# Optimization experiments

Hardware: AMD Instinct MI355X
Metric: run time of the kernel (lower is better)

The kernel has to match this reference:

```python
import jax, jax.numpy as jnp
import numpy as np

B, T, D, H = 64, 512, 1024, 1024


def setup_inputs() -> dict:
    key = jax.random.key(0)
    k1, k2, k3, k4, k5, k6 = jax.random.split(key, 6)
    feature = jax.random.normal(k1, (B, T, D), dtype=jnp.float32)
    # lengths sorted descending (pack_padded_sequence enforce_sorted=True); max == T
    lens = jnp.sort(jax.random.randint(k2, (B,), 1, T + 1))[::-1]
    seq_len = lens.at[0].set(T).astype(jnp.int32)
    s = 1.0 / np.sqrt(H)
    W_ih = jax.random.uniform(k3, (4 * H, D), jnp.float32, -s, s)
    W_hh = jax.random.uniform(k4, (4 * H, H), jnp.float32, -s, s)
    b_ih = jax.random.uniform(k5, (4 * H,), jnp.float32, -s, s)
    b_hh = jax.random.uniform(k6, (4 * H,), jnp.float32, -s, s)
    return {"feature": feature, "W_ih": W_ih, "W_hh": W_hh,
            "b_ih": b_ih, "b_hh": b_hh, "seq_len": seq_len}


def _lstm(feature, W_ih, W_hh, b_ih, b_hh, seq_len):
    Bb, Tt, _ = feature.shape
    Hh = W_hh.shape[1]
    # precompute input contributions for all steps: [B,T,4H] -> [T,B,4H]
    x_gates = jnp.einsum('btd,gd->btg', feature, W_ih) + (b_ih + b_hh)
    x_gates = jnp.transpose(x_gates, (1, 0, 2))
    # valid-step mask per timestep: [T,B]
    mask = (jnp.arange(Tt)[:, None] < seq_len[None, :])

    def step(carry, inp):
        h, c = carry
        xg, m = inp  # [B,4H], [B]
        gates = xg + h @ W_hh.T
        i, f, g, o = jnp.split(gates, 4, axis=-1)  # PyTorch gate order i,f,g,o
        i = jax.nn.sigmoid(i)
        f = jax.nn.sigmoid(f)
        g = jnp.tanh(g)
        o = jax.nn.sigmoid(o)
        c_new = f * c + i * g
        h_new = o * jnp.tanh(c_new)
        m = m[:, None]
        h = jnp.where(m, h_new, h)  # packed semantics: state frozen past length
        c = jnp.where(m, c_new, c)
        out = jnp.where(m, h_new, 0.0)  # pad_packed_sequence pads with zeros
        return (h, c), out

    h0 = jnp.zeros((Bb, Hh), feature.dtype)
    c0 = jnp.zeros((Bb, Hh), feature.dtype)
    _, outs = jax.lax.scan(step, (h0, c0), (x_gates, mask))
    return jnp.transpose(outs, (1, 0, 2))  # [B,T,H]


def reference(feature, W_ih, W_hh, b_ih, b_hh, seq_len):
    return _lstm(feature, W_ih, W_hh, b_ih, b_hh, seq_len)
```

## Files before the change

kernel.cpp:

```cpp
#include <hip/hip_runtime.h>
#include <stdint.h>

typedef unsigned short ushort_t;
typedef unsigned long long ull_t;
typedef __attribute__((ext_vector_type(8))) short short8;
typedef __attribute__((ext_vector_type(2))) unsigned long long ull2;
typedef __attribute__((ext_vector_type(4))) float f32x4;
typedef __attribute__((ext_vector_type(4))) float float4v;
typedef __attribute__((ext_vector_type(4))) unsigned short ushort4v;
typedef __attribute__((ext_vector_type(4))) unsigned int uint4v;

#define NB 64
#define NT 512
#define ND 1024
#define NHH 1024
#define NG 4096

__device__ __forceinline__ ushort_t f2bf(float x) {
    uint32_t u = __builtin_bit_cast(uint32_t, x);
    u += 0x7fffu + ((u >> 16) & 1u);
    return (ushort_t)(u >> 16);
}
__device__ __forceinline__ float bf2f(ushort_t b) {
    uint32_t u = ((uint32_t)b) << 16;
    return __builtin_bit_cast(float, u);
}
__device__ __forceinline__ float fsigmoid(float x) { return 1.f / (1.f + __expf(-x)); }
__device__ __forceinline__ float ftanh(float x) {
    float ax = __builtin_fabsf(x);
    float e = __expf(-2.f * ax);
    float r = (1.f - e) / (1.f + e);
    return x < 0.f ? -r : r;
}
__device__ __forceinline__ void xg_store(float* p, float v) { *p = v; }
__device__ __forceinline__ void xg_store(ushort_t* p, float v) { *p = f2bf(v); }
__device__ __forceinline__ float4v xg_load4(const float4v* p) { return *p; }
__device__ __forceinline__ float4v xg_load4(const ushort4v* p) {
    ushort4v u = *p;
    float4v r = { bf2f(u[0]), bf2f(u[1]), bf2f(u[2]), bf2f(u[3]) };
    return r;
}
__device__ __forceinline__ void async_cp16(const ushort_t* g, ushort_t* s) {
    __builtin_amdgcn_global_load_lds(
        (const __attribute__((address_space(1))) uint32_t*)g,
        (__attribute__((address_space(3))) uint32_t*)s, 16, 0, 0);
}

__global__ __launch_bounds__(256) void k_prep(
    const float* __restrict__ feat, const float* __restrict__ wih,
    const float* __restrict__ whh,
    ushort_t* __restrict__ featb, ushort_t* __restrict__ wihb,
    ushort_t* __restrict__ whhb, ushort_t* __restrict__ hbuf,
    int* __restrict__ cnt)
{
    const size_t NF = (size_t)NB * NT * ND / 4;
    const size_t NW = (size_t)NG * ND / 4;
    const size_t NHB = (size_t)2 * 65536 * 2 / 16;
    size_t total = NF + 2 * NW + NHB;
    size_t stride = (size_t)gridDim.x * blockDim.x;
    for (size_t i = (size_t)blockIdx.x * blockDim.x + threadIdx.x; i < total; i += stride) {
        if (i < NF) {
            float4v v = ((const float4v*)feat)[i];
            ushort4v o = { f2bf(v[0]), f2bf(v[1]), f2bf(v[2]), f2bf(v[3]) };
            ((ushort4v*)featb)[i] = o;
        } else if (i < NF + NW) {
            size_t j = i - NF;
            size_t row = j >> 8, kc = j & 255;
            size_t rowp = ((row & 1023) << 2) | (row >> 10);
            float4v v = ((const float4v*)wih)[j];
            ushort4v o = { f2bf(v[0]), f2bf(v[1]), f2bf(v[2]), f2bf(v[3]) };
            ((ushort4v*)wihb)[rowp * 256 + kc] = o;
        } else if (i < NF + 2 * NW) {
            size_t j = i - NF - NW;
            float4v v = ((const float4v*)whh)[j];
            ushort4v o = { f2bf(v[0]), f2bf(v[1]), f2bf(v[2]), f2bf(v[3]) };
            ((ushort4v*)whhb)[j] = o;
        } else {
            size_t j = i - NF - 2 * NW;
            uint4v z = { 0u, 0u, 0u, 0u };
            ((uint4v*)hbuf)[j] = z;
        }
    }
    if (blockIdx.x < 16) cnt[blockIdx.x * 256 + threadIdx.x] = 0;
}

template <typename XGT>
__global__ __launch_bounds__(256) void k_gemm(
    const ushort_t* __restrict__ Ab,
    const ushort_t* __restrict__ Bb,
    const float* __restrict__ bih, const float* __restrict__ bhh,
    const int* __restrict__ slenp, XGT* __restrict__ xg)
{
    int bid = blockIdx.x;
    int panel = bid >> 8;
    int qq = bid & 255;
    int mt = (panel << 3) | (qq & 7);
    int nt = qq >> 3;
    int m0 = mt << 7, n0 = nt << 7;
    int b = m0 >> 9;
    int t0 = m0 & 511;
    int sl = slenp[b];
    if (t0 >= sl) return;

    __shared__ short8 ldsA8[1024];
    __shared__ short8 ldsB8[1024];
    ushort_t* ldsA = (ushort_t*)ldsA8;
    ushort_t* ldsB = (ushort_t*)ldsB8;
    const ushort_t* gA = Ab + (size_t)m0 * 1024;
    const ushort_t* gB = Bb + (size_t)n0 * 1024;

    int tid = threadIdx.x;
    int wave = tid >> 6, lane = tid & 63;
    int wm = (wave >> 1) << 6;
    int wn = (wave & 1) << 6;
    int fl = lane & 15, fq = lane >> 4;

    f32x4 acc[4][4];
#pragma unroll
    for (int i = 0; i < 4; i++)
#pragma unroll
        for (int j = 0; j < 4; j++) { f32x4 z = {0.f, 0.f, 0.f, 0.f}; acc[i][j] = z; }

    int srow_[4], skb_[4];
#pragma unroll
    for (int u = 0; u < 4; u++) {
        int s = u * 256 + tid;
        srow_[u] = s >> 3;
        skb_[u] = (s & 7) ^ (srow_[u] & 7);
    }

    for (int k0 = 0; k0 < 1024; k0 += 64) {
        if (k0) __syncthreads();
#pragma unroll
        for (int u = 0; u < 4; u++) {
            ushort_t* sa = ldsA + (size_t)(u * 256 + wave * 64) * 8;
            ushort_t* sb = ldsB + (size_t)(u * 256 + wave * 64) * 8;
            async_cp16(gA + (size_t)srow_[u] * 1024 + k0 + skb_[u] * 8, sa);
            async_cp16(gB + (size_t)srow_[u] * 1024 + k0 + skb_[u] * 8, sb);
        }
        __syncthreads();
#pragma unroll
        for (int ks = 0; ks < 2; ks++) {
            int kc = ks * 4 + fq;
            short8 af[4], bf[4];
#pragma unroll
            for (int i = 0; i < 4; i++) {
                int ra = wm + i * 16 + fl;
                int rb = wn + i * 16 + fl;
                af[i] = ldsA8[ra * 8 + (kc ^ (ra & 7))];
                bf[i] = ldsB8[rb * 8 + (kc ^ (rb & 7))];
            }
#pragma unroll
            for (int i = 0; i < 4; i++)
#pragma unroll
                for (int j = 0; j < 4; j++)
                    acc[i][j] = __builtin_amdgcn_mfma_f32_16x16x32_bf16(af[i], bf[j], acc[i][j], 0, 0, 0);
        }
    }
#pragma unroll
    for (int j = 0; j < 4; j++) {
        int rp = n0 + wn + j * 16 + fl;
        int bi = ((rp & 3) << 10) | (rp >> 2);
        float bv = bih[bi] + bhh[bi];
#pragma unroll
        for (int i = 0; i < 4; i++) {
#pragma unroll
            for (int r = 0; r < 4; r++) {
                int m = wm + i * 16 + fq * 4 + r;
                int t = t0 + m;
                if (t < sl)
                    xg_store(&xg[((size_t)t * 64 + b) * 4096 + rp], acc[i][j][r] + bv);
            }
        }
    }
}

template <typename XG4>
__global__ __launch_bounds__(256, 1) void k_rec(
    const ushort_t* __restrict__ whhb, const XG4* __restrict__ xg4,
    const int* __restrict__ slenp, ushort_t* __restrict__ hbuf,
    float* __restrict__ out, int* __restrict__ cnt)
{
    const int tid = threadIdx.x;
    const int ks = tid >> 6, lane = tid & 63;
    const int wg = blockIdx.x;
    const int mb = wg >> 6;
    const int mem = wg & 63;
    const int j0 = mem << 4;
    const int nn = lane & 15, q = lane >> 4;

    short8 wfrag[4][8];
    {
        const short8* w8 = (const short8*)whhb;
#pragma unroll
        for (int g = 0; g < 4; g++) {
            const short8* wp = w8 + (size_t)(g * NHH + j0 + nn) * 128 + ks * 32;
#pragma unroll
            for (int u = 0; u < 8; u++) wfrag[g][u] = wp[u * 4 + q];
        }
    }
    const int eb = tid >> 4, ej = tid & 15;
    const int b_g = (mb << 4) + eb;
    const int j_g = j0 + ej;
    const int slen = slenp[b_g];
    const int blk_len = slenp[mb << 4];
    const int ab = (mb << 4) + nn;

    int* flags = cnt + mb * 1024;
    int* myflag = flags + mem * 16 + ks * 4;
    const int* pollp = flags + ((ks * 16 + (lane >> 2)) * 16) + (lane & 3) * 4;

    __shared__ float red[4 * 16 * 84];

    float c_st = 0.f, h_st = 0.f, hv_prev = 0.f;
    float4v xv = { 0.f, 0.f, 0.f, 0.f };
    if (0 < slen) xv = xg_load4(&xg4[(size_t)b_g * 1024 + j_g]);

#pragma unroll 1
    for (int t = 0; t < blk_len; ++t) {
        if (t > 0) out[((size_t)b_g * NT + (t - 1)) * 1024 + j_g] = hv_prev;
        float4v nxv = { 0.f, 0.f, 0.f, 0.f };
        if (t + 1 < slen) nxv = xg_load4(&xg4[((size_t)(t + 1) * 64 + b_g) * 1024 + j_g]);

        if (t > 0) {
            while (true) {
                int f = __hip_atomic_load(pollp, __ATOMIC_RELAXED, __HIP_MEMORY_SCOPE_AGENT);
                if (__ballot(f >= t) == ~0ull) break;
            }
            asm volatile("" ::: "memory");
        }

        const ull_t* hb8 = (const ull_t*)(hbuf + (size_t)(t & 1) * 65536);
        ull_t raw[16];
#pragma unroll
        for (int u = 0; u < 8; u++) {
            size_t ch = ((size_t)((ks * 32 + u * 4 + q) * 64 + ab)) * 2;
            raw[2 * u]     = __hip_atomic_load(&hb8[ch],     __ATOMIC_RELAXED, __HIP_MEMORY_SCOPE_AGENT);
            raw[2 * u + 1] = __hip_atomic_load(&hb8[ch + 1], __ATOMIC_RELAXED, __HIP_MEMORY_SCOPE_AGENT);
        }
        f32x4 acc[4];
#pragma unroll
        for (int g = 0; g < 4; g++) { f32x4 z = {0.f, 0.f, 0.f, 0.f}; acc[g] = z; }
#pragma unroll
        for (int u = 0; u < 8; u++) {
            ull2 p; p[0] = raw[2 * u]; p[1] = raw[2 * u + 1];
            short8 af = __builtin_bit_cast(short8, p);
#pragma unroll
            for (int g = 0; g < 4; g++)
                acc[g] = __builtin_amdgcn_mfma_f32_16x16x32_bf16(af, wfrag[g][u], acc[g], 0, 0, 0);
        }
        __syncthreads();
#pragma unroll
        for (int g = 0; g < 4; g++)
            *(f32x4*)&red[g * 1344 + nn * 84 + ks * 20 + q * 4] = acc[g];
        __syncthreads();

        float hv = 0.f;
        if (t < slen) {
            float s[4];
#pragma unroll
            for (int g = 0; g < 4; g++) {
                const float* rp = &red[g * 1344 + ej * 84 + eb];
                s[g] = (rp[0] + rp[20]) + (rp[40] + rp[60]);
            }
            float ip = s[0] + xv[0];
            float fp = s[1] + xv[1];
            float gp = s[2] + xv[2];
            float op = s[3] + xv[3];
            float i_s = fsigmoid(ip), f_s = fsigmoid(fp);
            float g_t = ftanh(gp), o_s = fsigmoid(op);
            float cn = __builtin_fmaf(f_s, c_st, i_s * g_t);
            c_st = cn;
            h_st = o_s * ftanh(cn);
            hv = h_st;
        }
        hv_prev = hv;
        __hip_atomic_store(&hbuf[(size_t)((t + 1) & 1) * 65536 +
                                 (size_t)((j_g >> 3) * 64 + b_g) * 8 + (j_g & 7)],
                           f2bf(h_st), __ATOMIC_RELAXED, __HIP_MEMORY_SCOPE_AGENT);
        xv = nxv;
        asm volatile("s_waitcnt vmcnt(0)" ::: "memory");
        if (lane == 0)
            __hip_atomic_store(myflag, t + 1, __ATOMIC_RELAXED, __HIP_MEMORY_SCOPE_AGENT);
    }
    out[((size_t)b_g * NT + (blk_len - 1)) * 1024 + j_g] = hv_prev;
    for (int t = blk_len; t < NT; ++t)
        out[((size_t)b_g * NT + t) * 1024 + j_g] = 0.f;
}

extern "C" void kernel_launch(void* const* d_in, const int* in_sizes, int n_in,
                              void* d_out, int out_size, void* d_ws, size_t ws_size,
                              hipStream_t stream)
{
    const float* feat = (const float*)d_in[0];
    const float* wih  = (const float*)d_in[1];
    const float* whh  = (const float*)d_in[2];
    const float* bih  = (const float*)d_in[3];
    const float* bhh  = (const float*)d_in[4];
    const int*   sl   = (const int*)d_in[5];
    float* out = (float*)d_out;
    char* ws = (char*)d_ws;

    size_t off = 0;
    auto take = [&](size_t bytes) -> size_t {
        size_t o = off; off += (bytes + 255) & ~(size_t)255; return o;
    };
    size_t o_featb = take((size_t)NB * NT * ND * 2);
    size_t o_wihb  = take((size_t)NG * ND * 2);
    size_t o_whhb  = take((size_t)NG * ND * 2);
    size_t o_hbuf  = take((size_t)2 * 65536 * 2);
    size_t o_cnt   = take(16384);
    size_t o_xg    = off;

    ushort_t* featb = (ushort_t*)(ws + o_featb);
    ushort_t* wihb  = (ushort_t*)(ws + o_wihb);
    ushort_t* whhb  = (ushort_t*)(ws + o_whhb);
    ushort_t* hbuf  = (ushort_t*)(ws + o_hbuf);
    int* cnt        = (int*)(ws + o_cnt);

    k_prep<<<2048, 256, 0, stream>>>(feat, wih, whh, featb, wihb, whhb, hbuf, cnt);

    size_t xg_elems = (size_t)NT * NB * NG;
    bool f32xg = (o_xg + xg_elems * 4) <= ws_size;
    if (f32xg) {
        float* xg = (float*)(ws + o_xg);
        k_gemm<float><<<8192, 256, 0, stream>>>(featb, wihb, bih, bhh, sl, xg);
        k_rec<float4v><<<256, 256, 0, stream>>>(whhb, (const float4v*)xg, sl, hbuf, out, cnt);
    } else {
        ushort_t* xg = (ushort_t*)(ws + o_xg);
        k_gemm<ushort_t><<<8192, 256, 0, stream>>>(featb, wihb, bih, bhh, sl, xg);
        k_rec<ushort4v><<<256, 256, 0, stream>>>(whhb, (const ushort4v*)xg, sl, hbuf, out, cnt);
    }
}
```

Baseline: 2.119 ms.

## Halve recurrent workgroups, stage h in LDS, and simplify flag polling

The recurrent kernel now runs 128 workgroups of 512 threads instead of 256 of 256. Each workgroup covers 32 hidden units across two 16-column wave groups, so fewer groups take part in the per-step global barrier. The hidden state is loaded from global memory once per workgroup with coalesced loads, staged in LDS and shared by all eight waves, instead of each wave doing its own strided global loads. Flag polling becomes a per-thread 64-bit load with a bounded spin instead of a wavefront ballot. Output stores are written in the same step rather than deferred, and the spin guard risks silently wrong results if it ever times out.

```diff
diff --git a/kernel.cpp b/kernel.cpp
--- a/kernel.cpp
+++ b/kernel.cpp
@@ -176,83 +176,100 @@
 }
 
 template <typename XG4>
-__global__ __launch_bounds__(256, 1) void k_rec(
+__global__ __launch_bounds__(512, 2) void k_rec(
     const ushort_t* __restrict__ whhb, const XG4* __restrict__ xg4,
     const int* __restrict__ slenp, ushort_t* __restrict__ hbuf,
     float* __restrict__ out, int* __restrict__ cnt)
 {
     const int tid = threadIdx.x;
-    const int ks = tid >> 6, lane = tid & 63;
     const int wg = blockIdx.x;
-    const int mb = wg >> 6;
-    const int mem = wg & 63;
-    const int j0 = mem << 4;
+    const int mb = wg >> 5;
+    const int mem = wg & 31;
+    const int j0 = mem << 5;
+    const int w = tid >> 6, lane = tid & 63;
+    const int jb = w >> 2, ks = w & 3;
     const int nn = lane & 15, q = lane >> 4;
 
     short8 wfrag[4][8];
     {
         const short8* w8 = (const short8*)whhb;
+        const int jw = j0 + (jb << 4);
 #pragma unroll
         for (int g = 0; g < 4; g++) {
-            const short8* wp = w8 + (size_t)(g * NHH + j0 + nn) * 128 + ks * 32;
+            const short8* wp = w8 + (size_t)(g * NHH + jw + nn) * 128 + ks * 32;
 #pragma unroll
             for (int u = 0; u < 8; u++) wfrag[g][u] = wp[u * 4 + q];
         }
     }
-    const int eb = tid >> 4, ej = tid & 15;
-    const int b_g = (mb << 4) + eb;
-    const int j_g = j0 + ej;
+
+    const int j_t = tid & 31, b_t = tid >> 5;
+    const int b_g = (mb << 4) + b_t;
+    const int j_gl = j0 + j_t;
     const int slen = slenp[b_g];
     const int blk_len = slenp[mb << 4];
-    const int ab = (mb << 4) + nn;
-
-    int* flags = cnt + mb * 1024;
-    int* myflag = flags + mem * 16 + ks * 4;
-    const int* pollp = flags + ((ks * 16 + (lane >> 2)) * 16) + (lane & 3) * 4;
-
-    __shared__ float red[4 * 16 * 84];
-
-    float c_st = 0.f, h_st = 0.f, hv_prev = 0.f;
+
+    const int jc = tid >> 2, q4 = tid & 3;
+    const size_t src_base = ((size_t)(jc * 64 + (mb << 4) + (q4 << 2))) << 1;
+
+    int* flags = cnt + mb * 256;
+    const ull_t* flagsU = (const ull_t*)flags;
+    const int pollU = (jc >> 2) * 4 + q4;
+    const int myflag = mem * 8 + w;
+
+    __shared__ short8 A_lds8[2048];
+    __shared__ float red[4 * 2176];
+
+    float c_st = 0.f, h_st = 0.f;
     float4v xv = { 0.f, 0.f, 0.f, 0.f };
-    if (0 < slen) xv = xg_load4(&xg4[(size_t)b_g * 1024 + j_g]);
+    if (0 < slen) xv = xg_load4(&xg4[(size_t)b_g * 1024 + j_gl]);
 
 #pragma unroll 1
     for (int t = 0; t < blk_len; ++t) {
-        if (t > 0) out[((size_t)b_g * NT + (t - 1)) * 1024 + j_g] = hv_prev;
         float4v nxv = { 0.f, 0.f, 0.f, 0.f };
-        if (t + 1 < slen) nxv = xg_load4(&xg4[((size_t)(t + 1) * 64 + b_g) * 1024 + j_g]);
+        if (t + 1 < slen) nxv = xg_load4(&xg4[((size_t)(t + 1) * 64 + b_g) * 1024 + j_gl]);
 
         if (t > 0) {
+            int guard = 0;
             while (true) {
-                int f = __hip_atomic_load(pollp, __ATOMIC_RELAXED, __HIP_MEMORY_SCOPE_AGENT);
-                if (__ballot(f >= t) == ~0ull) break;
+                ull_t f = __hip_atomic_load(&flagsU[pollU], __ATOMIC_RELAXED, __HIP_MEMORY_SCOPE_AGENT);
+                if ((int)(uint32_t)f >= t && (int)(uint32_t)(f >> 32) >= t) break;
+                if (++guard > (1 << 20)) break;
             }
             asm volatile("" ::: "memory");
         }
-
-        const ull_t* hb8 = (const ull_t*)(hbuf + (size_t)(t & 1) * 65536);
-        ull_t raw[16];
+        const ull_t* src = (const ull_t*)(hbuf + (size_t)(t & 1) * 65536) + src_base;
+        ull_t v[8];
+#pragma unroll
+        for (int u2 = 0; u2 < 8; u2++)
+            v[u2] = __hip_atomic_load(&src[u2], __ATOMIC_RELAXED, __HIP_MEMORY_SCOPE_AGENT);
+#pragma unroll
+        for (int i = 0; i < 4; i++) {
+            ull2 p; p[0] = v[2 * i]; p[1] = v[2 * i + 1];
+            A_lds8[tid * 4 + i] = __builtin_bit_cast(short8, p);
+        }
+        __syncthreads();
+
+        f32x4 acc0 = { 0.f, 0.f, 0.f, 0.f };
+        f32x4 acc1 = acc0, acc2 = acc0, acc3 = acc0;
 #pragma unroll
         for (int u = 0; u < 8; u++) {
-            size_t ch = ((size_t)((ks * 32 + u * 4 + q) * 64 + ab)) * 2;
-            raw[2 * u]     = __hip_atomic_load(&hb8[ch],     __ATOMIC_RELAXED, __HIP_MEMORY_SCOPE_AGENT);
-            raw[2 * u + 1] = __hip_atomic_load(&hb8[ch + 1], __ATOMIC_RELAXED, __HIP_MEMORY_SCOPE_AGENT);
-        }
-        f32x4 acc[4];
-#pragma unroll
-        for (int g = 0; g < 4; g++) { f32x4 z = {0.f, 0.f, 0.f, 0.f}; acc[g] = z; }
-#pragma unroll
-        for (int u = 0; u < 8; u++) {
-            ull2 p; p[0] = raw[2 * u]; p[1] = raw[2 * u + 1];
-            short8 af = __builtin_bit_cast(short8, p);
-#pragma unroll
-            for (int g = 0; g < 4; g++)
-                acc[g] = __builtin_amdgcn_mfma_f32_16x16x32_bf16(af, wfrag[g][u], acc[g], 0, 0, 0);
-        }
-        __syncthreads();
-#pragma unroll
-        for (int g = 0; g < 4; g++)
-            *(f32x4*)&red[g * 1344 + nn * 84 + ks * 20 + q * 4] = acc[g];
+            short8 af = A_lds8[(ks * 32 + u * 4 + q) * 16 + nn];
+            acc0 = __builtin_amdgcn_mfma_f32_16x16x32_bf16(af, wfrag[0][u], acc0, 0, 0, 0);
+            acc1 = __builtin_amdgcn_mfma_f32_16x16x32_bf16(af, wfrag[1][u], acc1, 0, 0, 0);
+            acc2 = __builtin_amdgcn_mfma_f32_16x16x32_bf16(af, wfrag[2][u], acc2, 0, 0, 0);
+            acc3 = __builtin_amdgcn_mfma_f32_16x16x32_bf16(af, wfrag[3][u], acc3, 0, 0, 0);
+        }
+        {
+            const int jj = (jb << 4) + nn;
+#pragma unroll
+            for (int r = 0; r < 4; r++) {
+                int bo = jj * 68 + (q * 4 + r) * 4 + ks;
+                red[0 * 2176 + bo] = acc0[r];
+                red[1 * 2176 + bo] = acc1[r];
+                red[2 * 2176 + bo] = acc2[r];
+                red[3 * 2176 + bo] = acc3[r];
+            }
+        }
         __syncthreads();
 
         float hv = 0.f;
@@ -260,8 +277,8 @@
             float s[4];
 #pragma unroll
             for (int g = 0; g < 4; g++) {
-                const float* rp = &red[g * 1344 + ej * 84 + eb];
-                s[g] = (rp[0] + rp[20]) + (rp[40] + rp[60]);
+                f32x4 pv = *(const f32x4*)&red[g * 2176 + j_t * 68 + b_t * 4];
+                s[g] = (pv[0] + pv[1]) + (pv[2] + pv[3]);
             }
             float ip = s[0] + xv[0];
             float fp = s[1] + xv[1];
@@ -274,18 +291,17 @@
             h_st = o_s * ftanh(cn);
             hv = h_st;
         }
-        hv_prev = hv;
         __hip_atomic_store(&hbuf[(size_t)((t + 1) & 1) * 65536 +
-                                 (size_t)((j_g >> 3) * 64 + b_g) * 8 + (j_g & 7)],
+                                 (size_t)((j_gl >> 3) * 64 + b_g) * 8 + (j_gl & 7)],
                            f2bf(h_st), __ATOMIC_RELAXED, __HIP_MEMORY_SCOPE_AGENT);
-        xv = nxv;
         asm volatile("s_waitcnt vmcnt(0)" ::: "memory");
         if (lane == 0)
-            __hip_atomic_store(myflag, t + 1, __ATOMIC_RELAXED, __HIP_MEMORY_SCOPE_AGENT);
-    }
-    out[((size_t)b_g * NT + (blk_len - 1)) * 1024 + j_g] = hv_prev;
-    for (int t = blk_len; t < NT; ++t)
-        out[((size_t)b_g * NT + t) * 1024 + j_g] = 0.f;
+            __hip_atomic_store(&flags[myflag], t + 1, __ATOMIC_RELAXED, __HIP_MEMORY_SCOPE_AGENT);
+        out[((size_t)b_g * NT + t) * 1024 + j_gl] = hv;
+        xv = nxv;
+    }
+    for (int t2 = blk_len; t2 < NT; ++t2)
+        out[((size_t)b_g * NT + t2) * 1024 + j_gl] = 0.f;
 }
 
 extern "C" void kernel_launch(void* const* d_in, const int* in_sizes, int n_in,
@@ -325,10 +341,10 @@
     if (f32xg) {
         float* xg = (float*)(ws + o_xg);
         k_gemm<float><<<8192, 256, 0, stream>>>(featb, wihb, bih, bhh, sl, xg);
-        k_rec<float4v><<<256, 256, 0, stream>>>(whhb, (const float4v*)xg, sl, hbuf, out, cnt);
+        k_rec<float4v><<<128, 512, 0, stream>>>(whhb, (const float4v*)xg, sl, hbuf, out, cnt);
     } else {
         ushort_t* xg = (ushort_t*)(ws + o_xg);
         k_gemm<ushort_t><<<8192, 256, 0, stream>>>(featb, wihb, bih, bhh, sl, xg);
-        k_rec<ushort4v><<<256, 256, 0, stream>>>(whhb, (const ushort4v*)xg, sl, hbuf, out, cnt);
-    }
-}
+        k_rec<ushort4v><<<128, 512, 0, stream>>>(whhb, (const ushort4v*)xg, sl, hbuf, out, cnt);
+    }
+}
```

Result: slower. 2.903 ms (+37.0%).

## Fuse input-projection GEMM and recurrence into one persistent kernel with readiness flags

Applied to the files above, without the earlier changes.

Merges the xg GEMM and the recurrent LSTM kernel into a single launch. The first 256 blocks run the recurrence, and the remaining blocks compute GEMM tiles reordered by time window, bumping per-tile ready counters. The recurrence blocks poll those counters before consuming each 128-step window, so the serial recurrence can start before the full input projection finishes. This risks deadlock or contention if the recurrence blocks occupy CUs the GEMM blocks need, which the code guards with bounded spin loops. It also depends on block scheduling order and adds atomic stores on the GEMM output.

```diff
diff --git a/kernel.cpp b/kernel.cpp
--- a/kernel.cpp
+++ b/kernel.cpp
@@ -32,8 +32,12 @@
     float r = (1.f - e) / (1.f + e);
     return x < 0.f ? -r : r;
 }
-__device__ __forceinline__ void xg_store(float* p, float v) { *p = v; }
-__device__ __forceinline__ void xg_store(ushort_t* p, float v) { *p = f2bf(v); }
+__device__ __forceinline__ void xg_astore(float* p, float v) {
+    __hip_atomic_store(p, v, __ATOMIC_RELAXED, __HIP_MEMORY_SCOPE_AGENT);
+}
+__device__ __forceinline__ void xg_astore(ushort_t* p, float v) {
+    __hip_atomic_store(p, f2bf(v), __ATOMIC_RELAXED, __HIP_MEMORY_SCOPE_AGENT);
+}
 __device__ __forceinline__ float4v xg_load4(const float4v* p) { return *p; }
 __device__ __forceinline__ float4v xg_load4(const ushort4v* p) {
     ushort4v u = *p;
@@ -84,103 +88,116 @@
     if (blockIdx.x < 16) cnt[blockIdx.x * 256 + threadIdx.x] = 0;
 }
 
-template <typename XGT>
-__global__ __launch_bounds__(256) void k_gemm(
+template <typename XGT, typename XG4>
+__global__ __launch_bounds__(256, 2) void k_fused(
     const ushort_t* __restrict__ Ab,
     const ushort_t* __restrict__ Bb,
     const float* __restrict__ bih, const float* __restrict__ bhh,
-    const int* __restrict__ slenp, XGT* __restrict__ xg)
+    const int* __restrict__ slenp,
+    XGT* xg, const ushort_t* __restrict__ whhb,
+    ushort_t* hbuf, float* __restrict__ out, int* cnt)
 {
-    int bid = blockIdx.x;
-    int panel = bid >> 8;
-    int qq = bid & 255;
-    int mt = (panel << 3) | (qq & 7);
-    int nt = qq >> 3;
-    int m0 = mt << 7, n0 = nt << 7;
-    int b = m0 >> 9;
-    int t0 = m0 & 511;
-    int sl = slenp[b];
-    if (t0 >= sl) return;
-
-    __shared__ short8 ldsA8[1024];
-    __shared__ short8 ldsB8[1024];
-    ushort_t* ldsA = (ushort_t*)ldsA8;
-    ushort_t* ldsB = (ushort_t*)ldsB8;
-    const ushort_t* gA = Ab + (size_t)m0 * 1024;
-    const ushort_t* gB = Bb + (size_t)n0 * 1024;
-
-    int tid = threadIdx.x;
-    int wave = tid >> 6, lane = tid & 63;
-    int wm = (wave >> 1) << 6;
-    int wn = (wave & 1) << 6;
-    int fl = lane & 15, fq = lane >> 4;
-
-    f32x4 acc[4][4];
-#pragma unroll
-    for (int i = 0; i < 4; i++)
-#pragma unroll
-        for (int j = 0; j < 4; j++) { f32x4 z = {0.f, 0.f, 0.f, 0.f}; acc[i][j] = z; }
-
-    int srow_[4], skb_[4];
-#pragma unroll
-    for (int u = 0; u < 4; u++) {
-        int s = u * 256 + tid;
-        srow_[u] = s >> 3;
-        skb_[u] = (s & 7) ^ (srow_[u] & 7);
-    }
-
-    for (int k0 = 0; k0 < 1024; k0 += 64) {
-        if (k0) __syncthreads();
+    extern __shared__ char smem[];
+    int* rdy = cnt + 1024;
+
+    if (blockIdx.x >= 256) {
+        int bid2 = blockIdx.x - 256;
+        int w = bid2 >> 11;
+        int qq = bid2 & 2047;
+        int pp = qq >> 8;
+        int q2 = qq & 255;
+        int bl = (pp << 3) | (q2 & 7);
+        int nt = q2 >> 3;
+        int mt = (bl << 2) | w;
+        int m0 = mt << 7, n0 = nt << 7;
+        int b = bl;
+        int t0 = w << 7;
+        int sl = slenp[b];
+        if (t0 >= sl) {
+            if (threadIdx.x == 0)
+                __hip_atomic_fetch_add(&rdy[mt], 1, __ATOMIC_RELAXED, __HIP_MEMORY_SCOPE_AGENT);
+            return;
+        }
+
+        short8* ldsA8 = (short8*)smem;
+        short8* ldsB8 = (short8*)(smem + 16384);
+        ushort_t* ldsA = (ushort_t*)ldsA8;
+        ushort_t* ldsB = (ushort_t*)ldsB8;
+        const ushort_t* gA = Ab + (size_t)m0 * 1024;
+        const ushort_t* gB = Bb + (size_t)n0 * 1024;
+
+        int tid = threadIdx.x;
+        int wave = tid >> 6, lane = tid & 63;
+        int wm = (wave >> 1) << 6;
+        int wn = (wave & 1) << 6;
+        int fl = lane & 15, fq = lane >> 4;
+
+        f32x4 acc[4][4];
+#pragma unroll
+        for (int i = 0; i < 4; i++)
+#pragma unroll
+            for (int j = 0; j < 4; j++) { f32x4 z = {0.f, 0.f, 0.f, 0.f}; acc[i][j] = z; }
+
+        int srow_[4], skb_[4];
 #pragma unroll
         for (int u = 0; u < 4; u++) {
-            ushort_t* sa = ldsA + (size_t)(u * 256 + wave * 64) * 8;
-            ushort_t* sb = ldsB + (size_t)(u * 256 + wave * 64) * 8;
-            async_cp16(gA + (size_t)srow_[u] * 1024 + k0 + skb_[u] * 8, sa);
-            async_cp16(gB + (size_t)srow_[u] * 1024 + k0 + skb_[u] * 8, sb);
-        }
+            int s = u * 256 + tid;
+            srow_[u] = s >> 3;
+            skb_[u] = (s & 7) ^ (srow_[u] & 7);
+        }
+
+        for (int k0 = 0; k0 < 1024; k0 += 64) {
+            if (k0) __syncthreads();
+#pragma unroll
+            for (int u = 0; u < 4; u++) {
+                ushort_t* sa = ldsA + (size_t)(u * 256 + wave * 64) * 8;
+                ushort_t* sb = ldsB + (size_t)(u * 256 + wave * 64) * 8;
+                async_cp16(gA + (size_t)srow_[u] * 1024 + k0 + skb_[u] * 8, sa);
+                async_cp16(gB + (size_t)srow_[u] * 1024 + k0 + skb_[u] * 8, sb);
+            }
+            __syncthreads();
+#pragma unroll
+            for (int ks = 0; ks < 2; ks++) {
+                int kc = ks * 4 + fq;
+                short8 af[4], bf[4];
+#pragma unroll
+                for (int i = 0; i < 4; i++) {
+                    int ra = wm + i * 16 + fl;
+                    int rb = wn + i * 16 + fl;
+                    af[i] = ldsA8[ra * 8 + (kc ^ (ra & 7))];
+                    bf[i] = ldsB8[rb * 8 + (kc ^ (rb & 7))];
+                }
+#pragma unroll
+                for (int i = 0; i < 4; i++)
+#pragma unroll
+                    for (int j = 0; j < 4; j++)
+                        acc[i][j] = __builtin_amdgcn_mfma_f32_16x16x32_bf16(af[i], bf[j], acc[i][j], 0, 0, 0);
+            }
+        }
+#pragma unroll
+        for (int j = 0; j < 4; j++) {
+            int rp = n0 + wn + j * 16 + fl;
+            int bi = ((rp & 3) << 10) | (rp >> 2);
+            float bv = bih[bi] + bhh[bi];
+#pragma unroll
+            for (int i = 0; i < 4; i++) {
+#pragma unroll
+                for (int r = 0; r < 4; r++) {
+                    int m = wm + i * 16 + fq * 4 + r;
+                    int t = t0 + m;
+                    if (t < sl)
+                        xg_astore(&xg[((size_t)t * 64 + b) * 4096 + rp], acc[i][j][r] + bv);
+                }
+            }
+        }
+        asm volatile("s_waitcnt vmcnt(0)" ::: "memory");
         __syncthreads();
-#pragma unroll
-        for (int ks = 0; ks < 2; ks++) {
-            int kc = ks * 4 + fq;
-            short8 af[4], bf[4];
-#pragma unroll
-            for (int i = 0; i < 4; i++) {
-                int ra = wm + i * 16 + fl;
-                int rb = wn + i * 16 + fl;
-                af[i] = ldsA8[ra * 8 + (kc ^ (ra & 7))];
-                bf[i] = ldsB8[rb * 8 + (kc ^ (rb & 7))];
-            }
-#pragma unroll
-            for (int i = 0; i < 4; i++)
-#pragma unroll
-                for (int j = 0; j < 4; j++)
-                    acc[i][j] = __builtin_amdgcn_mfma_f32_16x16x32_bf16(af[i], bf[j], acc[i][j], 0, 0, 0);
-        }
-    }
-#pragma unroll
-    for (int j = 0; j < 4; j++) {
-        int rp = n0 + wn + j * 16 + fl;
-        int bi = ((rp & 3) << 10) | (rp >> 2);
-        float bv = bih[bi] + bhh[bi];
-#pragma unroll
-        for (int i = 0; i < 4; i++) {
-#pragma unroll
-            for (int r = 0; r < 4; r++) {
-                int m = wm + i * 16 + fq * 4 + r;
-                int t = t0 + m;
-                if (t < sl)
-                    xg_store(&xg[((size_t)t * 64 + b) * 4096 + rp], acc[i][j][r] + bv);
-            }
-        }
-    }
-}
-
-template <typename XG4>
-__global__ __launch_bounds__(256, 1) void k_rec(
-    const ushort_t* __restrict__ whhb, const XG4* __restrict__ xg4,
-    const int* __restrict__ slenp, ushort_t* __restrict__ hbuf,
-    float* __restrict__ out, int* __restrict__ cnt)
-{
+        if (threadIdx.x == 0)
+            __hip_atomic_fetch_add(&rdy[mt], 1, __ATOMIC_RELAXED, __HIP_MEMORY_SCOPE_AGENT);
+        return;
+    }
+
+    const XG4* xg4 = (const XG4*)xg;
     const int tid = threadIdx.x;
     const int ks = tid >> 6, lane = tid & 63;
     const int wg = blockIdx.x;
@@ -206,26 +223,42 @@
     const int blk_len = slenp[mb << 4];
     const int ab = (mb << 4) + nn;
 
-    int* flags = cnt + mb * 1024;
-    int* myflag = flags + mem * 16 + ks * 4;
-    const int* pollp = flags + ((ks * 16 + (lane >> 2)) * 16) + (lane & 3) * 4;
-
-    __shared__ float red[4 * 16 * 84];
+    int* flags = cnt + mb * 256;
+    int* myflag = flags + mem * 4 + ks;
+    const int* fp = flags + (ks * 16 + (lane >> 2)) * 4 + (lane & 3);
+
+    const int ridx = ((mb << 4) + (lane & 15)) << 2;
+    auto waitwin = [&](int w2) {
+        int guard = 0;
+        while (true) {
+            int f = __hip_atomic_load(&rdy[ridx + w2], __ATOMIC_RELAXED, __HIP_MEMORY_SCOPE_AGENT);
+            if (__ballot(f >= 32) == ~0ull) break;
+            if (++guard > (1 << 20)) break;
+            __builtin_amdgcn_s_sleep(8);
+        }
+        asm volatile("" ::: "memory");
+    };
+
+    float* red = (float*)smem;
 
     float c_st = 0.f, h_st = 0.f, hv_prev = 0.f;
+    waitwin(0);
     float4v xv = { 0.f, 0.f, 0.f, 0.f };
     if (0 < slen) xv = xg_load4(&xg4[(size_t)b_g * 1024 + j_g]);
 
 #pragma unroll 1
     for (int t = 0; t < blk_len; ++t) {
         if (t > 0) out[((size_t)b_g * NT + (t - 1)) * 1024 + j_g] = hv_prev;
+        if (t + 1 < blk_len && ((t + 1) & 127) == 0) waitwin((t + 1) >> 7);
         float4v nxv = { 0.f, 0.f, 0.f, 0.f };
         if (t + 1 < slen) nxv = xg_load4(&xg4[((size_t)(t + 1) * 64 + b_g) * 1024 + j_g]);
 
         if (t > 0) {
+            int guard = 0;
             while (true) {
-                int f = __hip_atomic_load(pollp, __ATOMIC_RELAXED, __HIP_MEMORY_SCOPE_AGENT);
+                int f = __hip_atomic_load(fp, __ATOMIC_RELAXED, __HIP_MEMORY_SCOPE_AGENT);
                 if (__ballot(f >= t) == ~0ull) break;
+                if (++guard > (1 << 20)) break;
             }
             asm volatile("" ::: "memory");
         }
@@ -264,10 +297,10 @@
                 s[g] = (rp[0] + rp[20]) + (rp[40] + rp[60]);
             }
             float ip = s[0] + xv[0];
-            float fp = s[1] + xv[1];
+            float fpv = s[1] + xv[1];
             float gp = s[2] + xv[2];
             float op = s[3] + xv[3];
-            float i_s = fsigmoid(ip), f_s = fsigmoid(fp);
+            float i_s = fsigmoid(ip), f_s = fsigmoid(fpv);
             float g_t = ftanh(gp), o_s = fsigmoid(op);
             float cn = __builtin_fmaf(f_s, c_st, i_s * g_t);
             c_st = cn;
@@ -278,10 +311,10 @@
         __hip_atomic_store(&hbuf[(size_t)((t + 1) & 1) * 65536 +
                                  (size_t)((j_g >> 3) * 64 + b_g) * 8 + (j_g & 7)],
                            f2bf(h_st), __ATOMIC_RELAXED, __HIP_MEMORY_SCOPE_AGENT);
-        xv = nxv;
         asm volatile("s_waitcnt vmcnt(0)" ::: "memory");
         if (lane == 0)
             __hip_atomic_store(myflag, t + 1, __ATOMIC_RELAXED, __HIP_MEMORY_SCOPE_AGENT);
+        xv = nxv;
     }
     out[((size_t)b_g * NT + (blk_len - 1)) * 1024 + j_g] = hv_prev;
     for (int t = blk_len; t < NT; ++t)
@@ -324,11 +357,11 @@
     bool f32xg = (o_xg + xg_elems * 4) <= ws_size;
     if (f32xg) {
         float* xg = (float*)(ws + o_xg);
-        k_gemm<float><<<8192, 256, 0, stream>>>(featb, wihb, bih, bhh, sl, xg);
-        k_rec<float4v><<<256, 256, 0, stream>>>(whhb, (const float4v*)xg, sl, hbuf, out, cnt);
+        k_fused<float, float4v><<<8448, 256, 32768, stream>>>(
+            featb, wihb, bih, bhh, sl, xg, whhb, hbuf, out, cnt);
     } else {
         ushort_t* xg = (ushort_t*)(ws + o_xg);
-        k_gemm<ushort_t><<<8192, 256, 0, stream>>>(featb, wihb, bih, bhh, sl, xg);
-        k_rec<ushort4v><<<256, 256, 0, stream>>>(whhb, (const ushort4v*)xg, sl, hbuf, out, cnt);
-    }
-}
+        k_fused<ushort_t, ushort4v><<<8448, 256, 32768, stream>>>(
+            featb, wihb, bih, bhh, sl, xg, whhb, hbuf, out, cnt);
+    }
+}
```

Measured after the change: 2.668 ms. 25.9% more time.

## Replace flag-based step barrier with parity bits embedded in bf16 hidden state

Applied to the files above, without the earlier changes.

The separate per-workgroup flag array and its polling barrier are removed. Instead, the lowest mantissa bit of each bf16 hidden-state element carries a step-parity tag, and readers spin on the data words themselves until every loaded chunk shows the expected parity. This drops the vmcnt wait, the flag store and the separate flag-poll round trip each timestep, so consumers can start as soon as their specific inputs arrive. In exchange the hidden state loses one mantissa bit of precision, the second buffer is initialised with the opposite parity, and a guard counter can break out of the spin and silently use stale data.

```diff
diff --git a/kernel.cpp b/kernel.cpp
--- a/kernel.cpp
+++ b/kernel.cpp
@@ -77,7 +77,8 @@
             ((ushort4v*)whhb)[j] = o;
         } else {
             size_t j = i - NF - 2 * NW;
-            uint4v z = { 0u, 0u, 0u, 0u };
+            uint32_t fill = (j < 8192) ? 0u : 0x00010001u;
+            uint4v z = { fill, fill, fill, fill };
             ((uint4v*)hbuf)[j] = z;
         }
     }
@@ -181,6 +182,7 @@
     const int* __restrict__ slenp, ushort_t* __restrict__ hbuf,
     float* __restrict__ out, int* __restrict__ cnt)
 {
+    (void)cnt;
     const int tid = threadIdx.x;
     const int ks = tid >> 6, lane = tid & 63;
     const int wg = blockIdx.x;
@@ -206,11 +208,9 @@
     const int blk_len = slenp[mb << 4];
     const int ab = (mb << 4) + nn;
 
-    int* flags = cnt + mb * 1024;
-    int* myflag = flags + mem * 16 + ks * 4;
-    const int* pollp = flags + ((ks * 16 + (lane >> 2)) * 16) + (lane & 3) * 4;
-
     __shared__ float red[4 * 16 * 84];
+
+    const ull_t TMASK = 0x0001000100010001ull;
 
     float c_st = 0.f, h_st = 0.f, hv_prev = 0.f;
     float4v xv = { 0.f, 0.f, 0.f, 0.f };
@@ -222,22 +222,40 @@
         float4v nxv = { 0.f, 0.f, 0.f, 0.f };
         if (t + 1 < slen) nxv = xg_load4(&xg4[((size_t)(t + 1) * 64 + b_g) * 1024 + j_g]);
 
-        if (t > 0) {
-            while (true) {
-                int f = __hip_atomic_load(pollp, __ATOMIC_RELAXED, __HIP_MEMORY_SCOPE_AGENT);
-                if (__ballot(f >= t) == ~0ull) break;
-            }
-            asm volatile("" ::: "memory");
-        }
-
         const ull_t* hb8 = (const ull_t*)(hbuf + (size_t)(t & 1) * 65536);
+        const ull_t texp = ((t >> 1) & 1) ? TMASK : 0ull;
         ull_t raw[16];
-#pragma unroll
-        for (int u = 0; u < 8; u++) {
-            size_t ch = ((size_t)((ks * 32 + u * 4 + q) * 64 + ab)) * 2;
-            raw[2 * u]     = __hip_atomic_load(&hb8[ch],     __ATOMIC_RELAXED, __HIP_MEMORY_SCOPE_AGENT);
-            raw[2 * u + 1] = __hip_atomic_load(&hb8[ch + 1], __ATOMIC_RELAXED, __HIP_MEMORY_SCOPE_AGENT);
-        }
+        uint32_t pend;
+        {
+            pend = 0xffffu;
+#pragma unroll
+            for (int u = 0; u < 8; u++) {
+                size_t ch = ((size_t)((ks * 32 + u * 4 + q) * 64 + ab)) * 2;
+                ull_t x0 = __hip_atomic_load(&hb8[ch],     __ATOMIC_RELAXED, __HIP_MEMORY_SCOPE_AGENT);
+                ull_t x1 = __hip_atomic_load(&hb8[ch + 1], __ATOMIC_RELAXED, __HIP_MEMORY_SCOPE_AGENT);
+                raw[2 * u] = x0; raw[2 * u + 1] = x1;
+                if ((x0 & TMASK) == texp) pend &= ~(1u << (2 * u));
+                if ((x1 & TMASK) == texp) pend &= ~(1u << (2 * u + 1));
+            }
+        }
+        int guard = 0;
+        while (pend) {
+            __builtin_amdgcn_s_sleep(1);
+#pragma unroll
+            for (int u = 0; u < 8; u++) {
+                size_t ch = ((size_t)((ks * 32 + u * 4 + q) * 64 + ab)) * 2;
+                if (pend & (1u << (2 * u))) {
+                    ull_t x = __hip_atomic_load(&hb8[ch], __ATOMIC_RELAXED, __HIP_MEMORY_SCOPE_AGENT);
+                    if ((x & TMASK) == texp) { raw[2 * u] = x; pend &= ~(1u << (2 * u)); }
+                }
+                if (pend & (1u << (2 * u + 1))) {
+                    ull_t x = __hip_atomic_load(&hb8[ch + 1], __ATOMIC_RELAXED, __HIP_MEMORY_SCOPE_AGENT);
+                    if ((x & TMASK) == texp) { raw[2 * u + 1] = x; pend &= ~(1u << (2 * u + 1)); }
+                }
+            }
+            if (++guard > (1 << 20)) break;
+        }
+
         f32x4 acc[4];
 #pragma unroll
         for (int g = 0; g < 4; g++) { f32x4 z = {0.f, 0.f, 0.f, 0.f}; acc[g] = z; }
@@ -275,13 +293,11 @@
             hv = h_st;
         }
         hv_prev = hv;
+        ushort_t hw = (ushort_t)((f2bf(h_st) & 0xFFFEu) | (uint32_t)(((t + 1) >> 1) & 1));
         __hip_atomic_store(&hbuf[(size_t)((t + 1) & 1) * 65536 +
                                  (size_t)((j_g >> 3) * 64 + b_g) * 8 + (j_g & 7)],
-                           f2bf(h_st), __ATOMIC_RELAXED, __HIP_MEMORY_SCOPE_AGENT);
+                           hw, __ATOMIC_RELAXED, __HIP_MEMORY_SCOPE_AGENT);
         xv = nxv;
-        asm volatile("s_waitcnt vmcnt(0)" ::: "memory");
-        if (lane == 0)
-            __hip_atomic_store(myflag, t + 1, __ATOMIC_RELAXED, __HIP_MEMORY_SCOPE_AGENT);
     }
     out[((size_t)b_g * NT + (blk_len - 1)) * 1024 + j_g] = hv_prev;
     for (int t = blk_len; t < NT; ++t)
```

Result: slower. 2.409 ms (+13.7%).
